# Kernel optimization log

Hardware: AMD Instinct MI355X
Metric: run time of the kernel (lower is better)

## Reference

```python
import jax, jax.numpy as jnp
import numpy as np

B, NX, NEQ, NINEQ = 1024, 64, 1, 128
NCON = NEQ + NINEQ
MAX_ITERS = 5
INT_REG = 1e-6


def chol_upper(M):
    # upper Cholesky factor U with M = U^T U
    return jnp.swapaxes(jnp.linalg.cholesky(M), -1, -2)


def cho_solve_upper(U, rhs):
    # solve (U^T U) x = rhs, U batched upper triangular
    y = jax.lax.linalg.triangular_solve(U, rhs, left_side=True, lower=False, transpose_a=True)
    return jax.lax.linalg.triangular_solve(U, y, left_side=True, lower=False, transpose_a=False)


def pre_factor_kkt(Q, G, A):
    GT = jnp.swapaxes(G, 1, 2)
    AT = jnp.swapaxes(A, 1, 2)
    U_Q = chol_upper(Q)
    invQ_GT = cho_solve_upper(U_Q, GT)          # [B, nx, nineq]
    R = jnp.matmul(G, invQ_GT)                   # [B, nineq, nineq]
    invQ_AT = cho_solve_upper(U_Q, AT)           # [B, nx, neq]
    A_invQ_AT = jnp.matmul(A, invQ_AT)           # [B, neq, neq]
    U11 = chol_upper(A_invQ_AT)
    G_invQ_AT = jnp.matmul(G, invQ_AT)           # [B, nineq, neq]
    U12 = jax.lax.linalg.triangular_solve(U11, jnp.swapaxes(G_invQ_AT, 1, 2), left_side=True, lower=False)
    U1 = jnp.concatenate((U11, U12), axis=2)     # [B, neq, ncon]
    R = R - jnp.matmul(jnp.swapaxes(U12, 1, 2), U12)
    return U_Q, U1, R


def factor_kkt(U1, R, d):
    # Schur complement factor; d: [B, nineq, 1]
    d_diag = (1.0 / d[..., 0])[:, :, None] * jnp.eye(NINEQ, dtype=d.dtype)[None]
    mat = chol_upper(R + d_diag + INT_REG * jnp.eye(NINEQ, dtype=d.dtype)[None])
    lower = jnp.concatenate((jnp.zeros((B, NINEQ, NEQ), d.dtype), mat), axis=2)
    return jnp.concatenate((U1, lower), axis=1)  # [B, ncon, ncon] upper triangular


def solve_kkt(U_Q, d, G, A, U_S, rx, rs, rz, ry):
    GT = jnp.swapaxes(G, 1, 2)
    AT = jnp.swapaxes(A, 1, 2)
    invQ_rx = cho_solve_upper(U_Q, rx)
    H = jnp.matmul(G, invQ_rx) + rs / d - rz
    H1 = jnp.matmul(A, invQ_rx) - ry
    H = jnp.concatenate((H1, H), axis=1)
    w = -cho_solve_upper(U_S, H)
    w_y = w[:, :NEQ, :]
    w_z = w[:, NEQ:, :]
    g1 = -rx - jnp.matmul(GT, w_z) - jnp.matmul(AT, w_y)
    g2 = -rs - w_z
    dx = cho_solve_upper(U_Q, g1)
    ds = g2 / d
    return dx, ds, w_z, w_y


def get_step(v, dv):
    a = -v / dv
    a = jnp.where(a > 0, a, jnp.inf)
    return jnp.min(a, axis=1)  # [B, 1]


def setup_inputs() -> dict:
    key = jax.random.key(0)
    ks = jax.random.split(key, 6)
    M = jax.random.normal(ks[0], (B, NX, NX), jnp.float32)
    Q = jnp.matmul(M, jnp.swapaxes(M, 1, 2)) / NX + 2.0 * jnp.eye(NX, dtype=jnp.float32)[None]
    p = jax.random.normal(ks[1], (B, NX, 1), jnp.float32)
    A = jax.random.normal(ks[2], (B, NEQ, NX), jnp.float32)
    G = jax.random.normal(ks[3], (B, NINEQ, NX), jnp.float32)
    x0 = jax.random.normal(ks[4], (B, NX, 1), jnp.float32)
    b = jnp.matmul(A, x0)
    h = jnp.matmul(G, x0) + jax.random.uniform(ks[5], (B, NINEQ, 1), jnp.float32) + 0.1
    return {"Q": Q, "p": p, "A": A, "b": b, "G": G, "h": h}


def reference(Q, p, A, b, G, h):
    GT = jnp.swapaxes(G, 1, 2)
    AT = jnp.swapaxes(A, 1, 2)
    U_Q, U1, R = pre_factor_kkt(Q, G, A)

    # primal-dual init
    d0 = jnp.ones((B, NINEQ, 1), Q.dtype)
    U_S0 = factor_kkt(U1, R, d0)
    x, s, z, y = solve_kkt(U_Q, d0, G, A, U_S0, p, jnp.zeros((B, NINEQ, 1), Q.dtype), -h, -b)
    min_s = jnp.min(s, axis=1)  # [B,1]
    min_z = jnp.min(z, axis=1)
    s = s + jnp.where(1.0 - min_s > 1.0, 1.0 - min_s, 0.0)[:, :, None]
    z = z + jnp.where(1.0 - min_z > 1.0, 1.0 - min_z, 0.0)[:, :, None]

    def body(carry, _):
        x, s, z, y = carry
        rx = jnp.matmul(GT, z) + jnp.matmul(Q, x) + p + jnp.matmul(AT, y)
        rs = z
        rz = jnp.matmul(G, x) + s - h
        ry = jnp.matmul(A, x) - b
        mu = jnp.sum(s * z, axis=1) / NINEQ  # [B,1]
        d = z / s
        U_S = factor_kkt(U1, R, d)
        dxa, dsa, dza, dya = solve_kkt(U_Q, d, G, A, U_S, rx, rs, rz, ry)
        alpha = 0.999 * jnp.minimum(jnp.minimum(get_step(z, dza), get_step(s, dsa)), 1.0)[:, :, None]
        s_p = s + alpha * dsa
        z_p = z + alpha * dza
        sig = (jnp.sum(s_p * z_p, axis=1) / jnp.sum(s * z, axis=1)) ** 3
        mu_sig = (-mu * sig)[:, :, None]
        non_zero = (mu_sig + dsa * dza) / s
        dxc, dsc, dzc, dyc = solve_kkt(U_Q, d, G, A, U_S, rx * 0, non_zero, rz * 0, ry * 0)
        dx, ds, dz, dy = dxa + dxc, dsa + dsc, dza + dzc, dya + dyc
        alpha = 0.999 * jnp.minimum(jnp.minimum(get_step(z, dz), get_step(s, ds)), 1.0)[:, :, None]
        return (x + alpha * dx, s + alpha * ds, z + alpha * dz, y + alpha * dy), None

    (x, s, z, y), _ = jax.lax.scan(body, (x, s, z, y), None, length=MAX_ITERS)
    return x
```

## Files before the change

### kernel.cpp

```cpp
#include <hip/hip_runtime.h>
#include <math.h>


#define NT  512
#define WST 130
#define T1O 4352
#define T1S 132
#define GCO 12800
#define GCS 132

struct __align__(16) Smem {
  float W[16640];
  float scr[2048];
  float x[64], rxv[64], g1[64], t[64], dxa[64];
  float s[128], z[128], rz[128], dsa[128], dza[128], u12[128], dd[128], H[128], Y[128];
  float Rdiag[128];
  float scalbuf[64];
  float scal[16];
};
static_assert(sizeof(Smem) <= 81920, "LDS must fit 2 blocks/CU");

enum { SC_H1 = 2, SC_U11I = 4, SC_RY = 5, SC_MU = 6,
       SC_ALPHA = 7, SC_MUSIG = 8, SC_Y = 9, SC_DYA = 10, SC_WY = 11,
       SC_MINS = 12, SC_MINZ = 13 };

__device__ __forceinline__ float wred_sum(float v) {
#pragma unroll
  for (int off = 32; off > 0; off >>= 1) v += __shfl_down(v, off);
  return v;
}
__device__ __forceinline__ float wred_min(float v) {
#pragma unroll
  for (int off = 32; off > 0; off >>= 1) v = fminf(v, __shfl_down(v, off));
  return v;
}
__device__ __forceinline__ float step_val(float v, float dv) {
  float a = -v / dv;
  return (a > 0.0f) ? a : __builtin_inff();
}
__device__ __forceinline__ constexpr int pk16(int i) {
  return i * 16 - ((i * (i - 1)) >> 1);
}


template<int RW>
__device__ __forceinline__ void elim_publish(Smem& sm, float (&Wt)[4][8],
                                             int q, int tc) {
  const int tcd = q >> 1;
  const int co = (q & 1) << 2;
  float L10 = 0, L20 = 0, L30 = 0, L21 = 0, L31 = 0, L32 = 0;
  float id0 = 0, id1 = 0, id2 = 0, id3 = 0;
  if (tc == tcd) {
    float D[4][4];
#pragma unroll
    for (int m = 0; m < 4; ++m)
#pragma unroll
      for (int c = 0; c < 4; ++c) D[m][c] = Wt[m][co + c];
    id0 = 1.0f / D[0][0];
    L10 = D[0][1] * id0; L20 = D[0][2] * id0; L30 = D[0][3] * id0;
#pragma unroll
    for (int c = 0; c < 4; ++c) {
      D[1][c] -= L10 * D[0][c]; D[2][c] -= L20 * D[0][c]; D[3][c] -= L30 * D[0][c];
    }
    id1 = 1.0f / D[1][1];
    L21 = D[1][2] * id1; L31 = D[1][3] * id1;
#pragma unroll
    for (int c = 0; c < 4; ++c) { D[2][c] -= L21 * D[1][c]; D[3][c] -= L31 * D[1][c]; }
    id2 = 1.0f / D[2][2];
    L32 = D[2][3] * id2;
#pragma unroll
    for (int c = 0; c < 4; ++c) D[3][c] -= L32 * D[2][c];
    id3 = 1.0f / D[3][3];
  }
  const int src = ((q & 3) << 4) + tcd;
  L10 = __shfl(L10, src); L20 = __shfl(L20, src); L30 = __shfl(L30, src);
  L21 = __shfl(L21, src); L31 = __shfl(L31, src); L32 = __shfl(L32, src);
#pragma unroll
  for (int c = 0; c < 8; ++c) {
    Wt[1][c] = fmaf(-L10, Wt[0][c], Wt[1][c]);
    Wt[2][c] = fmaf(-L20, Wt[0][c], Wt[2][c]);
    Wt[2][c] = fmaf(-L21, Wt[1][c], Wt[2][c]);
    Wt[3][c] = fmaf(-L30, Wt[0][c], Wt[3][c]);
    Wt[3][c] = fmaf(-L31, Wt[1][c], Wt[3][c]);
    Wt[3][c] = fmaf(-L32, Wt[2][c], Wt[3][c]);
  }
  const int pb = (q >> 1) & 1;
  float* pp = sm.scr + pb * (8 * RW) + (q & 1) * (4 * RW);
  const int j0 = tc << 3;
#pragma unroll
  for (int m = 0; m < 4; ++m) {
    *(float4*)&pp[m * RW + j0]     = make_float4(Wt[m][0], Wt[m][1], Wt[m][2], Wt[m][3]);
    *(float4*)&pp[m * RW + j0 + 4] = make_float4(Wt[m][4], Wt[m][5], Wt[m][6], Wt[m][7]);
  }
  if (tc == tcd) {
    float* sb = sm.scalbuf + pb * 8 + ((q & 1) << 2);
    sb[0] = id0; sb[1] = id1; sb[2] = id2; sb[3] = id3;
    sm.Y[(q << 2) + 0] = id0; sm.Y[(q << 2) + 1] = id1;
    sm.Y[(q << 2) + 2] = id2; sm.Y[(q << 2) + 3] = id3;
  }
}

template<int RW>
__device__ __forceinline__ void apply_panel4(Smem& sm, float (&Wt)[4][8],
                                             int pb, int half, int i0, int j0) {
  const float* pp = sm.scr + pb * (8 * RW) + half * (4 * RW);
  const float* sb = sm.scalbuf + pb * 8 + (half << 2);
#pragma unroll 1
  for (int mm = 0; mm < 4; ++mm) {
    const float idm = sb[mm];
    const float4 pv  = *(const float4*)&pp[mm * RW + i0];
    const float4 pj0 = *(const float4*)&pp[mm * RW + j0];
    const float4 pj1 = *(const float4*)&pp[mm * RW + j0 + 4];
    const float um0 = pv.x * idm, um1 = pv.y * idm;
    const float um2 = pv.z * idm, um3 = pv.w * idm;
    const float pjv[8] = {pj0.x, pj0.y, pj0.z, pj0.w, pj1.x, pj1.y, pj1.z, pj1.w};
#pragma unroll
    for (int c = 0; c < 8; ++c) {
      Wt[0][c] = fmaf(-um0, pjv[c], Wt[0][c]);
      Wt[1][c] = fmaf(-um1, pjv[c], Wt[1][c]);
      Wt[2][c] = fmaf(-um2, pjv[c], Wt[2][c]);
      Wt[3][c] = fmaf(-um3, pjv[c], Wt[3][c]);
    }
  }
}

template<int N, int RW, int ST>
__device__ void chol_rank8(Smem& sm, float (&Wt)[4][8], int act, int tid) {
  const int tr = tid >> 4, tc = tid & 15;
  const int i0 = tr << 2, j0 = tc << 3;
  constexpr int NP = N / 8;
#pragma unroll 1
  for (int P = 0; P < NP; ++P) {
    const int pb = P & 1;
    if (P > 0 && act && tr >= 2 * P) {
      apply_panel4<RW>(sm, Wt, pb ^ 1, 0, i0, j0);
      apply_panel4<RW>(sm, Wt, pb ^ 1, 1, i0, j0);
    }
    if ((tid >> 6) == (P >> 1)) {
      if (act && tr == 2 * P) elim_publish<RW>(sm, Wt, 2 * P, tc);
      __threadfence_block();
      if (act && tr == 2 * P + 1) {
        apply_panel4<RW>(sm, Wt, pb, 0, i0, j0);
        elim_publish<RW>(sm, Wt, 2 * P + 1, tc);
      }
    }
    __syncthreads();
  }
}

template<int ST>
__device__ __forceinline__ void write_U(Smem& sm, float (&Wt)[4][8], int act,
                                        int i0, int j0) {
  if (act && j0 + 7 >= i0) {
    float sqv[4];
#pragma unroll
    for (int m = 0; m < 4; ++m) sqv[m] = sqrtf(sm.Y[i0 + m]);
    if (j0 >= i0 + 3) {
#pragma unroll
      for (int m = 0; m < 4; ++m)
#pragma unroll
        for (int qq = 0; qq < 4; ++qq)
          *(float2*)&sm.W[(i0 + m) * ST + j0 + 2 * qq] =
              make_float2(Wt[m][2 * qq] * sqv[m], Wt[m][2 * qq + 1] * sqv[m]);
    } else {
#pragma unroll
      for (int m = 0; m < 4; ++m) {
        const int i = i0 + m;
#pragma unroll
        for (int c = 0; c < 8; ++c) {
          const int j = j0 + c;
          if (j >= i) sm.W[i * ST + j] = Wt[m][c] * sqv[m];
        }
      }
    }
  }
}

template<int N, int ST>
__device__ void trtri_fast(Smem& sm, int tid) {
  constexpr int NB = N >> 4;
  if (tid < NB * 16) {
    const int blk = tid >> 4, c = tid & 15;
    const float* D = sm.W + (blk << 4) * ST + (blk << 4);
    float vv[16];
#pragma unroll
    for (int i = 15; i >= 0; --i) {
      float acc = 0.0f;
      for (int k = i + 1; k < 16; ++k) acc += D[i * ST + k] * vv[k];
      const float di = D[i * ST + i];
      const float val = (i == c) ? (1.0f / di) : (-acc / di);
      vv[i] = (i <= c) ? val : 0.0f;
    }
#pragma unroll
    for (int i = 0; i < 16; ++i)
      if (i <= c) sm.scr[blk * 136 + pk16(i) + (c - i)] = vv[i];
  }
  __syncthreads();
  constexpr int NROWS = 16 * (NB * (NB - 1) / 2);
  if (tid < NROWS) {
    int J = 1, base = 0;
    while (base + 16 * J <= tid) { base += 16 * J; ++J; }
    const int k = tid - base, Jb = J << 4;
    float u[16], o[16];
    float2* wr = (float2*)&sm.W[k * ST + Jb];
#pragma unroll
    for (int q = 0; q < 8; ++q) { const float2 v = wr[q]; u[2*q] = v.x; u[2*q+1] = v.y; }
    const float* vd = sm.scr + J * 136;
#pragma unroll
    for (int c = 0; c < 16; ++c) {
      float acc = 0.0f;
#pragma unroll
      for (int jj = 0; jj <= c; ++jj) acc += u[jj] * vd[pk16(jj) + (c - jj)];
      o[c] = acc;
    }
#pragma unroll
    for (int q = 0; q < 8; ++q) wr[q] = make_float2(o[2*q], o[2*q+1]);
  } else {
    for (int idx = tid - NROWS; idx < 256; idx += NT - NROWS) {
      const int r = idx >> 4, c2 = idx & 15;
      if (c2 >= r) sm.W[r * ST + c2] = sm.scr[pk16(r) + (c2 - r)];
    }
  }
  for (int J = 1; J < NB; ++J) {
    __syncthreads();
    const int Jb = J << 4;
    const int nStrip = Jb << 2;
    float acc[4] = {0.0f, 0.0f, 0.0f, 0.0f};
    int wi = 0, wc = 0;
    if (tid < nStrip) {
      wi = tid >> 2; wc = (tid & 3) << 2;
      for (int k = wi; k < Jb; ++k) {
        const float v = sm.W[wi * ST + k];
        const float2 u0 = *(const float2*)&sm.W[k * ST + Jb + wc];
        const float2 u1 = *(const float2*)&sm.W[k * ST + Jb + wc + 2];
        acc[0] = fmaf(v, u0.x, acc[0]); acc[1] = fmaf(v, u0.y, acc[1]);
        acc[2] = fmaf(v, u1.x, acc[2]); acc[3] = fmaf(v, u1.y, acc[3]);
      }
      acc[0] = -acc[0]; acc[1] = -acc[1]; acc[2] = -acc[2]; acc[3] = -acc[3];
    } else if (tid < nStrip + 64) {
      const int l = tid - nStrip;
      const int r = l >> 2; wi = Jb + r; wc = (l & 3) << 2;
      const float* vp = sm.scr + J * 136 + pk16(r) - r;
#pragma unroll
      for (int q = 0; q < 4; ++q) {
        const int c = wc + q;
        acc[q] = (c >= r) ? vp[c] : 0.0f;
      }
    }
    __syncthreads();
    if (tid < nStrip) {
      *(float2*)&sm.W[wi * ST + Jb + wc]     = make_float2(acc[0], acc[1]);
      *(float2*)&sm.W[wi * ST + Jb + wc + 2] = make_float2(acc[2], acc[3]);
    } else if (tid < nStrip + 64) {
      const int r = wi - Jb;
#pragma unroll
      for (int q = 0; q < 4; ++q)
        if (wc + q >= r) sm.W[wi * ST + Jb + wc + q] = acc[q];
    }
  }
  __syncthreads();
}


__device__ __forceinline__ void elim_sweep(Smem& sm, float (&Wt)[4][8],
                                           int q, int tc) {
  const int tcd = q >> 1;
  const int co = (q & 1) << 2;
  float L10 = 0, L20 = 0, L30 = 0, L21 = 0, L31 = 0, L32 = 0;
  float id0 = 0, id1 = 0, id2 = 0, id3 = 0;
  if (tc == tcd) {
    float D[4][4];
#pragma unroll
    for (int m = 0; m < 4; ++m)
#pragma unroll
      for (int c = 0; c < 4; ++c) D[m][c] = Wt[m][co + c];
    id0 = 1.0f / D[0][0];
    L10 = D[0][1] * id0; L20 = D[0][2] * id0; L30 = D[0][3] * id0;
#pragma unroll
    for (int c = 0; c < 4; ++c) {
      D[1][c] -= L10 * D[0][c]; D[2][c] -= L20 * D[0][c]; D[3][c] -= L30 * D[0][c];
    }
    id1 = 1.0f / D[1][1];
    L21 = D[1][2] * id1; L31 = D[1][3] * id1;
#pragma unroll
    for (int c = 0; c < 4; ++c) { D[2][c] -= L21 * D[1][c]; D[3][c] -= L31 * D[1][c]; }
    id2 = 1.0f / D[2][2];
    L32 = D[2][3] * id2;
#pragma unroll
    for (int c = 0; c < 4; ++c) D[3][c] -= L32 * D[2][c];
    id3 = 1.0f / D[3][3];
  }
  const int src = ((q & 3) << 4) + tcd;
  L10 = __shfl(L10, src); L20 = __shfl(L20, src); L30 = __shfl(L30, src);
  L21 = __shfl(L21, src); L31 = __shfl(L31, src); L32 = __shfl(L32, src);
  id0 = __shfl(id0, src); id1 = __shfl(id1, src);
  id2 = __shfl(id2, src); id3 = __shfl(id3, src);
#pragma unroll
  for (int c = 0; c < 8; ++c) {
    Wt[1][c] = fmaf(-L10, Wt[0][c], Wt[1][c]);
    Wt[2][c] = fmaf(-L20, Wt[0][c], Wt[2][c]);
    Wt[2][c] = fmaf(-L21, Wt[1][c], Wt[2][c]);
    Wt[3][c] = fmaf(-L30, Wt[0][c], Wt[3][c]);
    Wt[3][c] = fmaf(-L31, Wt[1][c], Wt[3][c]);
    Wt[3][c] = fmaf(-L32, Wt[2][c], Wt[3][c]);
  }
  const int pb = (q >> 1) & 1;
  float* pp = sm.scr + pb * 1024 + (q & 1) * 512;
  const int j0 = tc << 3;
#pragma unroll
  for (int m = 0; m < 4; ++m) {
    *(float4*)&pp[m * 128 + j0]     = make_float4(Wt[m][0], Wt[m][1], Wt[m][2], Wt[m][3]);
    *(float4*)&pp[m * 128 + j0 + 4] = make_float4(Wt[m][4], Wt[m][5], Wt[m][6], Wt[m][7]);
  }
  if (tc == tcd) {
    float* sb = sm.scalbuf + 16 + pb * 24 + (q & 1) * 12;
    sb[0] = id0; sb[1] = id1; sb[2] = id2; sb[3] = id3;
    sb[4] = L10; sb[5] = L20; sb[6] = L30; sb[7] = L21; sb[8] = L31; sb[9] = L32;
  }
#pragma unroll
  for (int c = 0; c < 8; ++c) {
    const float t3 = id3 * Wt[3][c];
    const float t2 = id2 * Wt[2][c] - L32 * t3;
    const float t1v = id1 * Wt[1][c] - L21 * t2 - L31 * t3;
    const float t0 = id0 * Wt[0][c] - L10 * t1v - L20 * t2 - L30 * t3;
    Wt[0][c] = t0; Wt[1][c] = t1v; Wt[2][c] = t2; Wt[3][c] = t3;
  }
  if (tc == tcd) {
    const float m10 = -L10, m21 = -L21, m32 = -L32;
    const float m20 = -L20 + L21 * L10;
    const float m31 = -L31 + L32 * L21;
    const float m30 = -L30 + L31 * L10 + L32 * L20 - L32 * L21 * L10;
    const float P00 = id0 + id1*m10*m10 + id2*m20*m20 + id3*m30*m30;
    const float P01 = id1*m10 + id2*m20*m21 + id3*m30*m31;
    const float P02 = id2*m20 + id3*m30*m32;
    const float P03 = id3*m30;
    const float P11 = id1 + id2*m21*m21 + id3*m31*m31;
    const float P12 = id2*m21 + id3*m31*m32;
    const float P13 = id3*m31;
    const float P22 = id2 + id3*m32*m32;
    const float P23 = id3*m32;
    const float P33 = id3;
    Wt[0][co+0] = -P00; Wt[0][co+1] = -P01; Wt[0][co+2] = -P02; Wt[0][co+3] = -P03;
    Wt[1][co+0] = -P01; Wt[1][co+1] = -P11; Wt[1][co+2] = -P12; Wt[1][co+3] = -P13;
    Wt[2][co+0] = -P02; Wt[2][co+1] = -P12; Wt[2][co+2] = -P22; Wt[2][co+3] = -P23;
    Wt[3][co+0] = -P03; Wt[3][co+1] = -P13; Wt[3][co+2] = -P23; Wt[3][co+3] = -P33;
  }
}

__device__ __forceinline__ void apply_sweep(Smem& sm, float (&Wt)[4][8],
                                            int q, int i0, int j0, int tr, int tc,
                                            int skip_partner) {
  if (tr == q) return;
  if (skip_partner && !(q & 1) && tr == q + 1) return;
  const int pb = (q >> 1) & 1;
  const float* pp = sm.scr + pb * 1024 + (q & 1) * 512;
  const float* sb = sm.scalbuf + 16 + pb * 24 + (q & 1) * 12;
#pragma unroll 1
  for (int mm = 0; mm < 4; ++mm) {
    const float idm = sb[mm];
    const float4 pv  = *(const float4*)&pp[mm * 128 + i0];
    const float4 pj0 = *(const float4*)&pp[mm * 128 + j0];
    const float4 pj1 = *(const float4*)&pp[mm * 128 + j0 + 4];
    const float um0 = pv.x * idm, um1 = pv.y * idm;
    const float um2 = pv.z * idm, um3 = pv.w * idm;
    const float pjv[8] = {pj0.x, pj0.y, pj0.z, pj0.w, pj1.x, pj1.y, pj1.z, pj1.w};
#pragma unroll
    for (int c = 0; c < 8; ++c) {
      Wt[0][c] = fmaf(-um0, pjv[c], Wt[0][c]);
      Wt[1][c] = fmaf(-um1, pjv[c], Wt[1][c]);
      Wt[2][c] = fmaf(-um2, pjv[c], Wt[2][c]);
      Wt[3][c] = fmaf(-um3, pjv[c], Wt[3][c]);
    }
  }
  if (tc == (q >> 1)) {
    const int co = (q & 1) << 2;
    const float id0 = sb[0], id1 = sb[1], id2 = sb[2], id3 = sb[3];
    const float L10 = sb[4], L20 = sb[5], L30 = sb[6];
    const float L21 = sb[7], L31 = sb[8], L32 = sb[9];
#pragma unroll
    for (int r = 0; r < 4; ++r) {
      const float f0 = pp[0 * 128 + i0 + r];
      const float f1 = pp[1 * 128 + i0 + r];
      const float f2 = pp[2 * 128 + i0 + r];
      const float f3 = pp[3 * 128 + i0 + r];
      const float t3 = id3 * f3;
      const float t2 = id2 * f2 - L32 * t3;
      const float t1v = id1 * f1 - L21 * t2 - L31 * t3;
      const float t0 = id0 * f0 - L10 * t1v - L20 * t2 - L30 * t3;
      Wt[r][co+0] = t0; Wt[r][co+1] = t1v; Wt[r][co+2] = t2; Wt[r][co+3] = t3;
    }
  }
}

__device__ void sweep128(Smem& sm, float (&Wt)[4][8], int tid) {
  const int tr = tid >> 4, tc = tid & 15;
  const int i0 = tr << 2, j0 = tc << 3;
#pragma unroll 1
  for (int P = 0; P < 16; ++P) {
    if (P > 0) {
      apply_sweep(sm, Wt, 2 * P - 2, i0, j0, tr, tc, 1);
      apply_sweep(sm, Wt, 2 * P - 1, i0, j0, tr, tc, 1);
    }
    if ((tid >> 6) == (P >> 1)) {
      if (tr == 2 * P) elim_sweep(sm, Wt, 2 * P, tc);
      __threadfence_block();
      if (tr == 2 * P + 1) {
        apply_sweep(sm, Wt, 2 * P, i0, j0, tr, tc, 0);
        elim_sweep(sm, Wt, 2 * P + 1, tc);
      }
    }
    __syncthreads();
  }
  apply_sweep(sm, Wt, 30, i0, j0, tr, tc, 1);
  apply_sweep(sm, Wt, 31, i0, j0, tr, tc, 1);
}

__device__ void factor_S(Smem& sm, int init, int tid) {
  const int tr = tid >> 4, tc = tid & 15;
  const int i0 = tr << 2, j0 = tc << 3;
  float Wt[4][8];
#pragma unroll
  for (int m = 0; m < 4; ++m) {
    const int i = i0 + m;
#pragma unroll
    for (int c = 0; c < 8; ++c) {
      const int j = j0 + c;
      float v;
      if (i < j)      v = sm.W[j * WST + i];
      else if (i > j) v = sm.W[i * WST + j];
      else            v = sm.Rdiag[i] + (init ? 1.0f : sm.s[i] / sm.z[i]) + 1e-6f;
      Wt[m][c] = v;
    }
  }
  sweep128(sm, Wt, tid);
  if (j0 + 7 >= i0) {
    if (j0 >= i0 + 3) {
#pragma unroll
      for (int m = 0; m < 4; ++m)
#pragma unroll
        for (int qq = 0; qq < 4; ++qq)
          *(float2*)&sm.W[(i0 + m) * WST + j0 + 2 * qq] =
              make_float2(-Wt[m][2 * qq], -Wt[m][2 * qq + 1]);
    } else {
#pragma unroll
      for (int m = 0; m < 4; ++m) {
        const int i = i0 + m;
#pragma unroll
        for (int c = 0; c < 8; ++c) {
          const int j = j0 + c;
          if (j >= i) sm.W[i * WST + j] = -Wt[m][c];
        }
      }
    }
  }
  __syncthreads();
}

__device__ void solve_kkt(Smem& sm, const float* qreg, const float* Gb, const float* Ab,
                          int has_rx, const float* rx, const float* rs,
                          int has_rz, const float* rz, float ry,
                          float* dx_t, float* ds_t, float* dz_t, int dy_slot,
                          int accum, int tid) {
  const float u11i = sm.scal[SC_U11I];
  const int o8 = tid >> 3, seg = tid & 7;
  if (has_rx) {
    float acc = 0.0f;
#pragma unroll
    for (int c = 0; c < 8; ++c) acc += qreg[c] * rx[seg * 8 + c];
    acc += __shfl_down(acc, 4); acc += __shfl_down(acc, 2); acc += __shfl_down(acc, 1);
    if (seg == 0) sm.t[o8] = acc;
    __syncthreads();
  }
  {
    const int i = tid >> 2, q = tid & 3;
    float acc = 0.0f;
    if (has_rx) {
      const float* gr = Gb + (i << 6) + (q << 4);
#pragma unroll
      for (int kk = 0; kk < 16; kk += 4) {
        const float4 g4 = *(const float4*)(gr + kk);
        const float4 t4 = *(const float4*)&sm.t[(q << 4) + kk];
        acc += g4.x * t4.x + g4.y * t4.y + g4.z * t4.z + g4.w * t4.w;
      }
    }
    float h1v = 0.0f;
    if (has_rx && tid < 64) h1v = Ab[tid] * sm.t[tid];
    h1v = wred_sum(h1v);
    acc += __shfl_down(acc, 2); acc += __shfl_down(acc, 1);
    if (q == 0) {
      if (rs) acc += rs[i] / sm.dd[i];
      if (has_rz) acc -= rz[i];
      sm.H[i] = acc;
    }
    if (tid == 0) sm.scal[SC_H1] = h1v - ry;
  }
  __syncthreads();
  const float y1 = sm.scal[SC_H1] * u11i;
  {
    const int o = tid & 127, p = tid >> 7;
    float acc = 0.0f;
    for (int k = (p << 5); k < (p << 5) + 32; ++k) {
      const int lo = (k < o) ? k : o;
      const int hi = (k < o) ? o : k;
      acc += sm.W[lo * WST + hi] * (sm.H[k] - sm.u12[k] * y1);
    }
    sm.scr[(p << 7) + o] = acc;
  }
  __syncthreads();
  if (tid < 128)
    sm.H[tid] = -(sm.scr[tid] + sm.scr[128 + tid] + sm.scr[256 + tid] + sm.scr[384 + tid]);
  __syncthreads();
  if (tid < 256) {
    const int o = tid & 63, p = tid >> 6;
    float acc = 0.0f;
    for (int i = (p << 5); i < (p << 5) + 32; ++i) acc -= Gb[(i << 6) + o] * sm.H[i];
    sm.scr[(p << 6) + o] = acc;
  } else if (tid < 384) {
    const int i = tid - 256;
    const float wzv = sm.H[i];
    const float r = rs ? rs[i] : 0.0f;
    const float dsv = (-r - wzv) / sm.dd[i];
    if (accum) { ds_t[i] += dsv; dz_t[i] += wzv; }
    else       { ds_t[i] = dsv;  dz_t[i] = wzv; }
  } else if (tid < 448) {
    const int l = tid - 384;
    float v = sm.u12[l] * sm.H[l] + sm.u12[l + 64] * sm.H[l + 64];
    v = wred_sum(v);
    if (l == 0) {
      const float wyv = -(y1 + v) * u11i;
      if (accum) sm.scal[dy_slot] += wyv; else sm.scal[dy_slot] = wyv;
      sm.scal[SC_WY] = wyv;
    }
  }
  __syncthreads();
  const float wy = sm.scal[SC_WY];
  if (tid < 64) {
    float acc = sm.scr[tid] + sm.scr[64 + tid] + sm.scr[128 + tid] + sm.scr[192 + tid]
              - Ab[tid] * wy;
    if (has_rx) acc -= rx[tid];
    sm.g1[tid] = acc;
  }
  __syncthreads();
  {
    float acc = 0.0f;
#pragma unroll
    for (int c = 0; c < 8; ++c) acc += qreg[c] * sm.g1[seg * 8 + c];
    acc += __shfl_down(acc, 4); acc += __shfl_down(acc, 2); acc += __shfl_down(acc, 1);
    if (seg == 0) { if (accum) dx_t[o8] += acc; else dx_t[o8] = acc; }
  }
  __syncthreads();
}

__global__ __launch_bounds__(NT, 2)
void optnet_kernel(const float* __restrict__ Qg, const float* __restrict__ pg,
                   const float* __restrict__ Ag, const float* __restrict__ bg,
                   const float* __restrict__ Gg, const float* __restrict__ hg,
                   float* __restrict__ outg) {
  __shared__ Smem sm;
  const int bId = blockIdx.x;
  const int tid = threadIdx.x;
  const float* Qb = Qg + (size_t)bId * 4096;
  const float* pb = pg + (size_t)bId * 64;
  const float* Ab = Ag + (size_t)bId * 64;
  const float  bb = bg[bId];
  const float* Gb = Gg + (size_t)bId * 8192;
  const float* hb = hg + (size_t)bId * 128;

  for (int idx = tid; idx < 4096; idx += NT)
    sm.W[(idx >> 6) * 68 + (idx & 63)] = Qb[idx];
  if (tid < 128) sm.dd[tid] = 1.0f;
  __syncthreads();
  {
    const int tr = tid >> 4, tc = tid & 15;
    const int i0 = tr << 2, j0 = tc << 3;
    const int act = (tr < 16) && (tc < 8);
    float Wt[4][8];
    if (act) {
#pragma unroll
      for (int m = 0; m < 4; ++m)
#pragma unroll
        for (int c = 0; c < 8; ++c)
          Wt[m][c] = sm.W[(i0 + m) * 68 + j0 + c];
    }
    chol_rank8<64, 64, 68>(sm, Wt, act, tid);
    write_U<68>(sm, Wt, act, i0, j0);
  }
  __syncthreads();
  trtri_fast<64, 68>(sm, tid);
  for (int idx = tid; idx < 4096; idx += NT) {
    const int i = idx >> 6, j = idx & 63;
    if (i > j) sm.W[i * 68 + j] = 0.0f;
  }
  __syncthreads();
  float qreg[8];
  {
    const int o = tid >> 3, sgq = tid & 7;
#pragma unroll 1
    for (int c = 0; c < 8; ++c) {
      const int j = sgq * 8 + c;
      float acc = 0.0f;
      for (int k = 0; k < 64; ++k) acc += sm.W[o * 68 + k] * sm.W[j * 68 + k];
      qreg[c] = acc;
    }
  }
  if (tid < 64) {
    float acc = 0.0f;
    for (int m = 0; m < 64; ++m) acc += sm.W[m * 68 + tid] * Ab[m];
    sm.t[tid] = acc;
  }
  __syncthreads();
  if (tid < 64) {
    float v = sm.t[tid] * sm.t[tid];
    v = wred_sum(v);
    if (tid == 0) sm.scal[SC_U11I] = 1.0f / sqrtf(v);
  }
  __syncthreads();
  {
    const int kt = tid & 15, jt = tid >> 4;
    const int k0 = kt << 2, j0 = jt << 2;
    float t1a[4][4] = {};
    for (int mc = 0; mc < 64; mc += 16) {
      for (int idx = tid; idx < 2048; idx += NT) {
        const int j = idx >> 4, mm = idx & 15;
        sm.W[GCO + mm * GCS + j] = Gb[j * 64 + mc + mm];
      }
      __syncthreads();
#pragma unroll 2
      for (int mm = 0; mm < 16; ++mm) {
        const float4 v = *(const float4*)&sm.W[(mc + mm) * 68 + k0];
        const float4 g = *(const float4*)&sm.W[GCO + mm * GCS + j0];
        const float vv[4] = {v.x, v.y, v.z, v.w};
        const float gg[4] = {g.x, g.y, g.z, g.w};
#pragma unroll
        for (int a = 0; a < 4; ++a)
#pragma unroll
          for (int b2 = 0; b2 < 4; ++b2) t1a[a][b2] = fmaf(vv[a], gg[b2], t1a[a][b2]);
      }
      __syncthreads();
    }
#pragma unroll
    for (int a = 0; a < 4; ++a)
      *(float4*)&sm.W[T1O + (k0 + a) * T1S + j0] =
          make_float4(t1a[a][0], t1a[a][1], t1a[a][2], t1a[a][3]);
  }
  __syncthreads();
  {
    const int o = tid & 127, p = tid >> 7;
    float acc = 0.0f;
    for (int k = (p << 4); k < (p << 4) + 16; ++k)
      acc += sm.W[T1O + k * T1S + o] * sm.t[k];
    sm.scr[(p << 7) + o] = acc;
  }
  __syncthreads();
  if (tid < 128)
    sm.u12[tid] = (sm.scr[tid] + sm.scr[128 + tid] + sm.scr[256 + tid] + sm.scr[384 + tid])
                  * sm.scal[SC_U11I];
  __syncthreads();
  float racc[4][8];
  {
    const int tr = tid >> 4, tc = tid & 15;
    const int i0 = tr << 2, j0 = tc << 3;
#pragma unroll
    for (int m = 0; m < 4; ++m)
#pragma unroll
      for (int c = 0; c < 8; ++c) racc[m][c] = 0.0f;
#pragma unroll 2
    for (int k = 0; k < 64; ++k) {
      const float4 a  = *(const float4*)&sm.W[T1O + k * T1S + i0];
      const float4 b0 = *(const float4*)&sm.W[T1O + k * T1S + j0];
      const float4 b1 = *(const float4*)&sm.W[T1O + k * T1S + j0 + 4];
      const float av[4] = {a.x, a.y, a.z, a.w};
      const float bv[8] = {b0.x, b0.y, b0.z, b0.w, b1.x, b1.y, b1.z, b1.w};
#pragma unroll
      for (int m = 0; m < 4; ++m)
#pragma unroll
        for (int c = 0; c < 8; ++c) racc[m][c] = fmaf(av[m], bv[c], racc[m][c]);
    }
#pragma unroll
    for (int m = 0; m < 4; ++m) {
      const float ui = sm.u12[i0 + m];
#pragma unroll
      for (int c = 0; c < 8; ++c) racc[m][c] -= ui * sm.u12[j0 + c];
    }
  }
  __syncthreads();
  {
    const int tr = tid >> 4, tc = tid & 15;
    const int i0 = tr << 2, j0 = tc << 3;
#pragma unroll
    for (int m = 0; m < 4; ++m) {
      const int i = i0 + m;
#pragma unroll
      for (int c = 0; c < 8; ++c) {
        const int j = j0 + c;
        if (i < j)       sm.W[j * WST + i] = racc[m][c];
        else if (i == j) sm.Rdiag[i] = racc[m][c];
      }
    }
  }
  if (tid < 128) sm.rz[tid] = -hb[tid];
  __syncthreads();

  factor_S(sm, 1, tid);
  solve_kkt(sm, qreg, Gb, Ab, 1, pb, nullptr, 1, sm.rz, -bb,
            sm.x, sm.s, sm.z, SC_Y, 0, tid);
  if (tid < 64) {
    float v = fminf(sm.s[tid], sm.s[tid + 64]);
    v = wred_min(v);
    if (tid == 0) sm.scal[SC_MINS] = v;
  } else if (tid < 128) {
    const int l = tid - 64;
    float v = fminf(sm.z[l], sm.z[l + 64]);
    v = wred_min(v);
    if (l == 0) sm.scal[SC_MINZ] = v;
  }
  __syncthreads();
  if (tid < 128) {
    const float cs = 1.0f - sm.scal[SC_MINS];
    if (cs > 1.0f) sm.s[tid] += cs;
  } else if (tid < 256) {
    const int i = tid - 128;
    const float cz = 1.0f - sm.scal[SC_MINZ];
    if (cz > 1.0f) sm.z[i] += cz;
  }
  __syncthreads();

  for (int it = 0; it < 5; ++it) {
    if (tid < 256) {
      const int o = tid & 63, pq = tid >> 6;
      float acc = 0.0f;
      for (int i = (pq << 5); i < (pq << 5) + 32; ++i) acc += Gb[(i << 6) + o] * sm.z[i];
      for (int k = (pq << 4); k < (pq << 4) + 16; ++k) acc += Qb[(k << 6) + o] * sm.x[k];
      sm.scr[(pq << 6) + o] = acc;
    } else {
      const int l = tid - 256, i = l >> 1, q = l & 1;
      const float* gr = Gb + (i << 6) + (q << 5);
      float acc = 0.0f;
#pragma unroll
      for (int kk = 0; kk < 32; kk += 4) {
        const float4 g4 = *(const float4*)(gr + kk);
        const float4 x4 = *(const float4*)&sm.x[(q << 5) + kk];
        acc += g4.x * x4.x + g4.y * x4.y + g4.z * x4.z + g4.w * x4.w;
      }
      acc += __shfl_down(acc, 1);
      if (q == 0) sm.rz[i] = acc + sm.s[i] - hb[i];
    }
    __syncthreads();
    if (tid < 64) {
      sm.rxv[tid] = pb[tid] + Ab[tid] * sm.scal[SC_Y]
                  + sm.scr[tid] + sm.scr[64 + tid] + sm.scr[128 + tid] + sm.scr[192 + tid];
    } else if (tid < 128) {
      const int l = tid - 64;
      float v = Ab[l] * sm.x[l];
      v = wred_sum(v);
      if (l == 0) sm.scal[SC_RY] = v - bb;
    } else if (tid < 192) {
      const int l = tid - 128;
      float v = sm.s[l] * sm.z[l] + sm.s[l + 64] * sm.z[l + 64];
      v = wred_sum(v);
      if (l == 0) sm.scal[SC_MU] = v * (1.0f / 128.0f);
    } else if (tid < 320) {
      const int i = tid - 192;
      sm.dd[i] = sm.z[i] / sm.s[i];
    }
    __syncthreads();
    factor_S(sm, 0, tid);
    solve_kkt(sm, qreg, Gb, Ab, 1, sm.rxv, sm.z, 1, sm.rz, sm.scal[SC_RY],
              sm.dxa, sm.dsa, sm.dza, SC_DYA, 0, tid);
    if (tid < 64) {
      float m = __builtin_inff();
#pragma unroll
      for (int rep = 0; rep < 2; ++rep) {
        const int i = tid + 64 * rep;
        m = fminf(m, step_val(sm.z[i], sm.dza[i]));
        m = fminf(m, step_val(sm.s[i], sm.dsa[i]));
      }
      m = wred_min(m);
      if (tid == 0) sm.scal[SC_ALPHA] = 0.999f * fminf(m, 1.0f);
    }
    __syncthreads();
    {
      const float alpha = sm.scal[SC_ALPHA];
      if (tid < 64) {
        float v = 0.0f;
#pragma unroll
        for (int rep = 0; rep < 2; ++rep) {
          const int i = tid + 64 * rep;
          v += (sm.s[i] + alpha * sm.dsa[i]) * (sm.z[i] + alpha * sm.dza[i]);
        }
        v = wred_sum(v);
        if (tid == 0) {
          const float mu = sm.scal[SC_MU];
          const float r = v / (mu * 128.0f);
          sm.scal[SC_MUSIG] = -mu * r * r * r;
        }
      }
    }
    __syncthreads();
    if (tid < 128)
      sm.rz[tid] = (sm.scal[SC_MUSIG] + sm.dsa[tid] * sm.dza[tid]) / sm.s[tid];
    __syncthreads();
    solve_kkt(sm, qreg, Gb, Ab, 0, nullptr, sm.rz, 0, nullptr, 0.0f,
              sm.dxa, sm.dsa, sm.dza, SC_DYA, 1, tid);
    if (tid < 64) {
      float m = __builtin_inff();
#pragma unroll
      for (int rep = 0; rep < 2; ++rep) {
        const int i = tid + 64 * rep;
        m = fminf(m, step_val(sm.z[i], sm.dza[i]));
        m = fminf(m, step_val(sm.s[i], sm.dsa[i]));
      }
      m = wred_min(m);
      if (tid == 0) sm.scal[SC_ALPHA] = 0.999f * fminf(m, 1.0f);
    }
    __syncthreads();
    {
      const float a2 = sm.scal[SC_ALPHA];
      if (tid < 128) sm.s[tid] += a2 * sm.dsa[tid];
      else if (tid < 256) sm.z[tid - 128] += a2 * sm.dza[tid - 128];
    }
    if (tid < 64) sm.x[tid] += sm.scal[SC_ALPHA] * sm.dxa[tid];
    if (tid == 64) sm.scal[SC_Y] += sm.scal[SC_ALPHA] * sm.scal[SC_DYA];
    __syncthreads();
  }
  if (tid < 64) outg[((size_t)bId << 6) + tid] = sm.x[tid];
}

extern "C" void kernel_launch(void* const* d_in, const int* in_sizes, int n_in,
                              void* d_out, int out_size, void* d_ws, size_t ws_size,
                              hipStream_t stream) {
  (void)n_in; (void)d_ws; (void)ws_size; (void)out_size;
  const float* Q = (const float*)d_in[0];
  const float* p = (const float*)d_in[1];
  const float* A = (const float*)d_in[2];
  const float* b = (const float*)d_in[3];
  const float* G = (const float*)d_in[4];
  const float* h = (const float*)d_in[5];
  const int B = in_sizes[3];
  optnet_kernel<<<B, NT, 0, stream>>>(Q, p, A, b, G, h, (float*)d_out);
}
```

Before: 2.420 ms.

## Cut block barriers by fusing reductions into consumers and using wave-local broadcasts

Removes several __syncthreads by recomputing the w_z partial sums inline in each consumer instead of materialising H and g1, and by replacing shared-memory scalar round-trips (alpha, min s/z) with wave shuffles in a single wave. The corrector's H is precomputed in the caller so the has_rx=0 path skips its first phase entirely. The G^T product in prefactorisation now reads G directly from global memory instead of staging chunks in LDS, which removes barriers there. The trade-off is redundant LDS reads for the recomputed sums and uncached-stride global loads of G.

```diff
diff --git a/kernel.cpp b/kernel.cpp
--- a/kernel.cpp
+++ b/kernel.cpp
@@ -6,8 +6,6 @@
 #define WST 130
 #define T1O 4352
 #define T1S 132
-#define GCO 12800
-#define GCS 132
 
 struct __align__(16) Smem {
   float W[16640];
@@ -21,8 +19,7 @@
 static_assert(sizeof(Smem) <= 81920, "LDS must fit 2 blocks/CU");
 
 enum { SC_H1 = 2, SC_U11I = 4, SC_RY = 5, SC_MU = 6,
-       SC_ALPHA = 7, SC_MUSIG = 8, SC_Y = 9, SC_DYA = 10, SC_WY = 11,
-       SC_MINS = 12, SC_MINZ = 13 };
+       SC_MUSIG = 8, SC_Y = 9, SC_DYA = 10, SC_WY = 11 };
 
 __device__ __forceinline__ float wred_sum(float v) {
 #pragma unroll
@@ -453,7 +450,6 @@
       }
     }
   }
-  __syncthreads();
 }
 
 __device__ void solve_kkt(Smem& sm, const float* qreg, const float* Gb, const float* Ab,
@@ -464,17 +460,17 @@
   const float u11i = sm.scal[SC_U11I];
   const int o8 = tid >> 3, seg = tid & 7;
   if (has_rx) {
-    float acc = 0.0f;
-#pragma unroll
-    for (int c = 0; c < 8; ++c) acc += qreg[c] * rx[seg * 8 + c];
-    acc += __shfl_down(acc, 4); acc += __shfl_down(acc, 2); acc += __shfl_down(acc, 1);
-    if (seg == 0) sm.t[o8] = acc;
-    __syncthreads();
-  }
-  {
-    const int i = tid >> 2, q = tid & 3;
-    float acc = 0.0f;
-    if (has_rx) {
+    {
+      float acc = 0.0f;
+#pragma unroll
+      for (int c = 0; c < 8; ++c) acc += qreg[c] * rx[seg * 8 + c];
+      acc += __shfl_down(acc, 4); acc += __shfl_down(acc, 2); acc += __shfl_down(acc, 1);
+      if (seg == 0) sm.t[o8] = acc;
+    }
+    __syncthreads();
+    {
+      const int i = tid >> 2, q = tid & 3;
+      float acc = 0.0f;
       const float* gr = Gb + (i << 6) + (q << 4);
 #pragma unroll
       for (int kk = 0; kk < 16; kk += 4) {
@@ -482,19 +478,18 @@
         const float4 t4 = *(const float4*)&sm.t[(q << 4) + kk];
         acc += g4.x * t4.x + g4.y * t4.y + g4.z * t4.z + g4.w * t4.w;
       }
-    }
-    float h1v = 0.0f;
-    if (has_rx && tid < 64) h1v = Ab[tid] * sm.t[tid];
-    h1v = wred_sum(h1v);
-    acc += __shfl_down(acc, 2); acc += __shfl_down(acc, 1);
-    if (q == 0) {
-      if (rs) acc += rs[i] / sm.dd[i];
-      if (has_rz) acc -= rz[i];
-      sm.H[i] = acc;
-    }
-    if (tid == 0) sm.scal[SC_H1] = h1v - ry;
-  }
-  __syncthreads();
+      float h1v = (tid < 64) ? Ab[tid] * sm.t[tid] : 0.0f;
+      h1v = wred_sum(h1v);
+      acc += __shfl_down(acc, 2); acc += __shfl_down(acc, 1);
+      if (q == 0) {
+        if (rs) acc += rs[i] / sm.dd[i];
+        if (has_rz) acc -= rz[i];
+        sm.H[i] = acc;
+      }
+      if (tid == 0) sm.scal[SC_H1] = h1v - ry;
+    }
+    __syncthreads();
+  }
   const float y1 = sm.scal[SC_H1] * u11i;
   {
     const int o = tid & 127, p = tid >> 7;
@@ -507,24 +502,27 @@
     sm.scr[(p << 7) + o] = acc;
   }
   __syncthreads();
-  if (tid < 128)
-    sm.H[tid] = -(sm.scr[tid] + sm.scr[128 + tid] + sm.scr[256 + tid] + sm.scr[384 + tid]);
-  __syncthreads();
   if (tid < 256) {
     const int o = tid & 63, p = tid >> 6;
     float acc = 0.0f;
-    for (int i = (p << 5); i < (p << 5) + 32; ++i) acc -= Gb[(i << 6) + o] * sm.H[i];
-    sm.scr[(p << 6) + o] = acc;
+    for (int i = (p << 5); i < (p << 5) + 32; ++i) {
+      const float wzv = -(sm.scr[i] + sm.scr[128 + i] + sm.scr[256 + i] + sm.scr[384 + i]);
+      acc -= Gb[(i << 6) + o] * wzv;
+    }
+    sm.scr[512 + (p << 6) + o] = acc;
   } else if (tid < 384) {
     const int i = tid - 256;
-    const float wzv = sm.H[i];
+    const float wzv = -(sm.scr[i] + sm.scr[128 + i] + sm.scr[256 + i] + sm.scr[384 + i]);
     const float r = rs ? rs[i] : 0.0f;
     const float dsv = (-r - wzv) / sm.dd[i];
     if (accum) { ds_t[i] += dsv; dz_t[i] += wzv; }
     else       { ds_t[i] = dsv;  dz_t[i] = wzv; }
   } else if (tid < 448) {
     const int l = tid - 384;
-    float v = sm.u12[l] * sm.H[l] + sm.u12[l + 64] * sm.H[l + 64];
+    const float wa = -(sm.scr[l] + sm.scr[128 + l] + sm.scr[256 + l] + sm.scr[384 + l]);
+    const int l2 = l + 64;
+    const float wb = -(sm.scr[l2] + sm.scr[128 + l2] + sm.scr[256 + l2] + sm.scr[384 + l2]);
+    float v = sm.u12[l] * wa + sm.u12[l2] * wb;
     v = wred_sum(v);
     if (l == 0) {
       const float wyv = -(y1 + v) * u11i;
@@ -534,17 +532,16 @@
   }
   __syncthreads();
   const float wy = sm.scal[SC_WY];
-  if (tid < 64) {
-    float acc = sm.scr[tid] + sm.scr[64 + tid] + sm.scr[128 + tid] + sm.scr[192 + tid]
-              - Ab[tid] * wy;
-    if (has_rx) acc -= rx[tid];
-    sm.g1[tid] = acc;
-  }
-  __syncthreads();
   {
     float acc = 0.0f;
 #pragma unroll
-    for (int c = 0; c < 8; ++c) acc += qreg[c] * sm.g1[seg * 8 + c];
+    for (int c = 0; c < 8; ++c) {
+      const int j = seg * 8 + c;
+      float g1v = sm.scr[512 + j] + sm.scr[512 + 64 + j] + sm.scr[512 + 128 + j]
+                + sm.scr[512 + 192 + j] - Ab[j] * wy;
+      if (has_rx) g1v -= rx[j];
+      acc += qreg[c] * g1v;
+    }
     acc += __shfl_down(acc, 4); acc += __shfl_down(acc, 2); acc += __shfl_down(acc, 1);
     if (seg == 0) { if (accum) dx_t[o8] += acc; else dx_t[o8] = acc; }
   }
@@ -619,24 +616,24 @@
     const int kt = tid & 15, jt = tid >> 4;
     const int k0 = kt << 2, j0 = jt << 2;
     float t1a[4][4] = {};
-    for (int mc = 0; mc < 64; mc += 16) {
-      for (int idx = tid; idx < 2048; idx += NT) {
-        const int j = idx >> 4, mm = idx & 15;
-        sm.W[GCO + mm * GCS + j] = Gb[j * 64 + mc + mm];
-      }
-      __syncthreads();
-#pragma unroll 2
-      for (int mm = 0; mm < 16; ++mm) {
-        const float4 v = *(const float4*)&sm.W[(mc + mm) * 68 + k0];
-        const float4 g = *(const float4*)&sm.W[GCO + mm * GCS + j0];
+#pragma unroll 1
+    for (int m = 0; m < 64; m += 4) {
+      const float4 g0 = *(const float4*)&Gb[(j0 + 0) * 64 + m];
+      const float4 g1 = *(const float4*)&Gb[(j0 + 1) * 64 + m];
+      const float4 g2 = *(const float4*)&Gb[(j0 + 2) * 64 + m];
+      const float4 g3 = *(const float4*)&Gb[(j0 + 3) * 64 + m];
+      const float gr[4][4] = {{g0.x, g0.y, g0.z, g0.w}, {g1.x, g1.y, g1.z, g1.w},
+                              {g2.x, g2.y, g2.z, g2.w}, {g3.x, g3.y, g3.z, g3.w}};
+#pragma unroll
+      for (int i = 0; i < 4; ++i) {
+        const float4 v = *(const float4*)&sm.W[(m + i) * 68 + k0];
         const float vv[4] = {v.x, v.y, v.z, v.w};
-        const float gg[4] = {g.x, g.y, g.z, g.w};
 #pragma unroll
         for (int a = 0; a < 4; ++a)
 #pragma unroll
-          for (int b2 = 0; b2 < 4; ++b2) t1a[a][b2] = fmaf(vv[a], gg[b2], t1a[a][b2]);
-      }
-      __syncthreads();
+          for (int b2 = 0; b2 < 4; ++b2)
+            t1a[a][b2] = fmaf(vv[a], gr[b2][i], t1a[a][b2]);
+      }
     }
 #pragma unroll
     for (int a = 0; a < 4; ++a)
@@ -707,21 +704,16 @@
   if (tid < 64) {
     float v = fminf(sm.s[tid], sm.s[tid + 64]);
     v = wred_min(v);
-    if (tid == 0) sm.scal[SC_MINS] = v;
+    v = __shfl(v, 0);
+    const float cs = 1.0f - v;
+    if (cs > 1.0f) { sm.s[tid] += cs; sm.s[tid + 64] += cs; }
   } else if (tid < 128) {
     const int l = tid - 64;
     float v = fminf(sm.z[l], sm.z[l + 64]);
     v = wred_min(v);
-    if (l == 0) sm.scal[SC_MINZ] = v;
-  }
-  __syncthreads();
-  if (tid < 128) {
-    const float cs = 1.0f - sm.scal[SC_MINS];
-    if (cs > 1.0f) sm.s[tid] += cs;
-  } else if (tid < 256) {
-    const int i = tid - 128;
-    const float cz = 1.0f - sm.scal[SC_MINZ];
-    if (cz > 1.0f) sm.z[i] += cz;
+    v = __shfl(v, 0);
+    const float cz = 1.0f - v;
+    if (cz > 1.0f) { sm.z[l] += cz; sm.z[l + 64] += cz; }
   }
   __syncthreads();
 
@@ -776,29 +768,29 @@
         m = fminf(m, step_val(sm.s[i], sm.dsa[i]));
       }
       m = wred_min(m);
-      if (tid == 0) sm.scal[SC_ALPHA] = 0.999f * fminf(m, 1.0f);
-    }
-    __syncthreads();
-    {
-      const float alpha = sm.scal[SC_ALPHA];
-      if (tid < 64) {
-        float v = 0.0f;
-#pragma unroll
-        for (int rep = 0; rep < 2; ++rep) {
-          const int i = tid + 64 * rep;
-          v += (sm.s[i] + alpha * sm.dsa[i]) * (sm.z[i] + alpha * sm.dza[i]);
-        }
-        v = wred_sum(v);
-        if (tid == 0) {
-          const float mu = sm.scal[SC_MU];
-          const float r = v / (mu * 128.0f);
-          sm.scal[SC_MUSIG] = -mu * r * r * r;
-        }
-      }
-    }
-    __syncthreads();
-    if (tid < 128)
-      sm.rz[tid] = (sm.scal[SC_MUSIG] + sm.dsa[tid] * sm.dza[tid]) / sm.s[tid];
+      float alpha = 0.999f * fminf(m, 1.0f);
+      alpha = __shfl(alpha, 0);
+      float v = 0.0f;
+#pragma unroll
+      for (int rep = 0; rep < 2; ++rep) {
+        const int i = tid + 64 * rep;
+        v += (sm.s[i] + alpha * sm.dsa[i]) * (sm.z[i] + alpha * sm.dza[i]);
+      }
+      v = wred_sum(v);
+      if (tid == 0) {
+        const float mu = sm.scal[SC_MU];
+        const float r = v / (mu * 128.0f);
+        sm.scal[SC_MUSIG] = -mu * r * r * r;
+      }
+    }
+    __syncthreads();
+    if (tid < 128) {
+      const float v = (sm.scal[SC_MUSIG] + sm.dsa[tid] * sm.dza[tid]) / sm.s[tid];
+      sm.rz[tid] = v;
+      sm.H[tid] = v / sm.dd[tid];
+    } else if (tid == 128) {
+      sm.scal[SC_H1] = 0.0f;
+    }
     __syncthreads();
     solve_kkt(sm, qreg, Gb, Ab, 0, nullptr, sm.rz, 0, nullptr, 0.0f,
               sm.dxa, sm.dsa, sm.dza, SC_DYA, 1, tid);
@@ -811,16 +803,15 @@
         m = fminf(m, step_val(sm.s[i], sm.dsa[i]));
       }
       m = wred_min(m);
-      if (tid == 0) sm.scal[SC_ALPHA] = 0.999f * fminf(m, 1.0f);
-    }
-    __syncthreads();
-    {
-      const float a2 = sm.scal[SC_ALPHA];
-      if (tid < 128) sm.s[tid] += a2 * sm.dsa[tid];
-      else if (tid < 256) sm.z[tid - 128] += a2 * sm.dza[tid - 128];
-    }
-    if (tid < 64) sm.x[tid] += sm.scal[SC_ALPHA] * sm.dxa[tid];
-    if (tid == 64) sm.scal[SC_Y] += sm.scal[SC_ALPHA] * sm.scal[SC_DYA];
+      float a2 = 0.999f * fminf(m, 1.0f);
+      a2 = __shfl(a2, 0);
+      sm.s[tid]      += a2 * sm.dsa[tid];
+      sm.s[tid + 64] += a2 * sm.dsa[tid + 64];
+      sm.z[tid]      += a2 * sm.dza[tid];
+      sm.z[tid + 64] += a2 * sm.dza[tid + 64];
+      sm.x[tid]      += a2 * sm.dxa[tid];
+      if (tid == 0) sm.scal[SC_Y] += a2 * sm.scal[SC_DYA];
+    }
     __syncthreads();
   }
   if (tid < 64) outg[((size_t)bId << 6) + tid] = sm.x[tid];
```

Result: no change. 2.456 ms (+1.5%).
